# Kernel optimization log

Measured on AMD Instinct MI355X. Metric: run time of the kernel, lower is better.

The kernel has to match this reference:

```python
import jax, jax.numpy as jnp
import numpy as np

H = 2  # attention heads, concat=False -> mean over heads

def _gat(x, src, dst, eattr, W, a_s, a_d, We, a_e, b, N):
    # x: [N, Fin], W: [Fin, H*C], a_*: [H, C], We: [1, H*C], b: [C]
    C = W.shape[1] // H
    xh = (x @ W).reshape(N, H, C)                      # [N,H,C]
    al_s = jnp.einsum('nhc,hc->nh', xh, a_s)           # [N,H]
    al_d = jnp.einsum('nhc,hc->nh', xh, a_d)           # [N,H]
    eh = (eattr @ We).reshape(-1, H, C)                # [E,H,C]
    al_e = jnp.einsum('ehc,hc->eh', eh, a_e)           # [E,H]
    alpha = jax.nn.leaky_relu(al_s[src] + al_d[dst] + al_e, 0.2)
    # segment softmax over incoming edges of each dst node
    amax = jax.lax.stop_gradient(jax.ops.segment_max(alpha, dst, num_segments=N))
    ex = jnp.exp(alpha - amax[dst])
    den = jax.ops.segment_sum(ex, dst, num_segments=N)
    att = ex / (den[dst] + 1e-16)                      # [E,H]
    out = jax.ops.segment_sum(xh[src] * att[:, :, None], dst, num_segments=N)
    return out.mean(axis=1) + b                        # [N,C]


def setup_inputs() -> dict:
    key = jax.random.key(0)
    ks = jax.random.split(key, 24)
    N, E, Fin, Ch, NG = 50000, 800000, 5, 64, 64
    p = lambda k, shp: (jax.random.normal(k, shp, dtype=jnp.float32) * 0.1)
    inp = {
        'x': jax.random.normal(ks[0], (N, Fin), dtype=jnp.float32),
        'edge_index': jax.random.randint(ks[1], (2, E), 0, N),
        'edge_attr': jax.random.uniform(ks[2], (E, 1), dtype=jnp.float32),
        'batch': jnp.sort(jax.random.randint(ks[3], (N,), 0, NG)),
        'W1': p(ks[4], (Fin, H * Ch)), 'as1': p(ks[5], (H, Ch)), 'ad1': p(ks[6], (H, Ch)),
        'We1': p(ks[7], (1, H * Ch)), 'ae1': p(ks[8], (H, Ch)), 'b1': jnp.zeros((Ch,), jnp.float32),
        'W2': p(ks[9], (Ch, H * Ch)), 'as2': p(ks[10], (H, Ch)), 'ad2': p(ks[11], (H, Ch)),
        'We2': p(ks[12], (1, H * Ch)), 'ae2': p(ks[13], (H, Ch)), 'b2': jnp.zeros((Ch,), jnp.float32),
        'Wlin': p(ks[14], (Ch, 1)), 'blin': jnp.zeros((1,), jnp.float32),
    }
    return inp


def reference(x, edge_index, edge_attr, batch,
              W1, as1, ad1, We1, ae1, b1,
              W2, as2, ad2, We2, ae2, b2,
              Wlin, blin):
    N = x.shape[0]
    NG = 64
    src0, dst0 = edge_index[0], edge_index[1]
    # PyG GATConv add_self_loops=True, fill_value='mean': per-dst mean of edge_attr
    cnt = jax.ops.segment_sum(jnp.ones((src0.shape[0], 1), x.dtype), dst0, num_segments=N)
    loop_attr = jax.ops.segment_sum(edge_attr, dst0, num_segments=N) / jnp.maximum(cnt, 1.0)
    loops = jnp.arange(N)
    src = jnp.concatenate([src0, loops])
    dst = jnp.concatenate([dst0, loops])
    eattr = jnp.concatenate([edge_attr, loop_attr], axis=0)
    h = jax.nn.relu(_gat(x, src, dst, eattr, W1, as1, ad1, We1, ae1, b1, N))
    h = jax.nn.relu(_gat(h, src, dst, eattr, W2, as2, ad2, We2, ae2, b2, N))
    # global mean pool over graphs
    cntb = jax.ops.segment_sum(jnp.ones((N,), h.dtype), batch, num_segments=NG)
    pooled = jax.ops.segment_sum(h, batch, num_segments=NG) / jnp.maximum(cntb, 1.0)[:, None]
    return (pooled @ Wlin + blin).squeeze()
```

## Files before the change

kernel.cpp:

```cpp
#include <hip/hip_runtime.h>
#include <hip/hip_bf16.h>
#include <math.h>

typedef unsigned int u32;
typedef __attribute__((ext_vector_type(8))) short short8v;
typedef __attribute__((ext_vector_type(4))) float f32x4;

#define LRELU(a) ((a) > 0.f ? (a) : 0.2f * (a))

#define FIX_SCALE 67108864.0f
#define FIX_INV   (1.0f / 67108864.0f)
#define CNT_SHIFT 40
#define SUM_MASK  0xFFFFFFFFFFULL

__device__ __forceinline__ u32 f2bf(float f) {
    u32 u = __float_as_uint(f);
    return (u + 0x7fffu + ((u >> 16) & 1u)) >> 16;
}
__device__ __forceinline__ float bfl(u32 w) { return __uint_as_float(w << 16); }
__device__ __forceinline__ float bfh(u32 w) { return __uint_as_float(w & 0xffff0000u); }

#define RED(x) _Pragma("unroll") for (int m_ = 32; m_ >= 1; m_ >>= 1) x += __shfl_xor(x, m_);
#define REDMAX(x) _Pragma("unroll") for (int m_ = 32; m_ >= 1; m_ >>= 1) x = fmaxf(x, __shfl_xor(x, m_));
#define RED32(x) _Pragma("unroll") for (int m_ = 16; m_ >= 1; m_ >>= 1) x += __shfl_xor(x, m_);
#define REDMAX32(x) _Pragma("unroll") for (int m_ = 16; m_ >= 1; m_ >>= 1) x = fmaxf(x, __shfl_xor(x, m_));


__global__ void hist_pos_kernel(const int* __restrict__ dst, const float* __restrict__ eattr,
                                unsigned long long* __restrict__ hist, int* __restrict__ pos, int E) {
    int e = blockIdx.x * blockDim.x + threadIdx.x;
    if (e < E) {
        int d = dst[e];
        unsigned long long v = (1ULL << CNT_SHIFT) |
                               (unsigned long long)(eattr[e] * FIX_SCALE + 0.5f);
        unsigned long long old = atomicAdd(&hist[d], v);
        pos[e] = (int)(old >> CNT_SHIFT);
    }
}

__global__ __launch_bounds__(256) void scan_phase1(const unsigned long long* __restrict__ hist,
                                                   int* __restrict__ block_sum, int N) {
    int t = threadIdx.x;
    int n = blockIdx.x * 256 + t;
    int v = (n < N) ? (int)(hist[n] >> CNT_SHIFT) + 1 : 0;
    RED(v)
    __shared__ int ws[4];
    if ((t & 63) == 0) ws[t >> 6] = v;
    __syncthreads();
    if (t == 0) block_sum[blockIdx.x] = ws[0] + ws[1] + ws[2] + ws[3];
}

__global__ __launch_bounds__(1024) void scan_phase2(const int* __restrict__ block_sum,
                                                    int* __restrict__ block_off,
                                                    int* __restrict__ row_ptr, int B, int N) {
    __shared__ int s[1024];
    int t = threadIdx.x;
    int v = (t < B) ? block_sum[t] : 0;
    s[t] = v;
    __syncthreads();
    for (int off = 1; off < 1024; off <<= 1) {
        int u = (t >= off) ? s[t - off] : 0;
        __syncthreads();
        s[t] += u;
        __syncthreads();
    }
    if (t < B) block_off[t] = s[t] - v;
    if (t == 1023) row_ptr[N] = s[1023];
}

__global__ __launch_bounds__(256) void scan_phase3(const unsigned long long* __restrict__ hist,
                                                   const int* __restrict__ block_off,
                                                   int* __restrict__ row_ptr,
                                                   int2* __restrict__ col, int N) {
    int t = threadIdx.x;
    int lane = t & 63;
    int n = blockIdx.x * 256 + t;
    unsigned long long hv = (n < N) ? hist[n] : 0ULL;
    int c = (n < N) ? (int)(hv >> CNT_SHIFT) + 1 : 0;
    int v = c;
#pragma unroll
    for (int m = 1; m < 64; m <<= 1) {
        int u = __shfl_up(v, m);
        if (lane >= m) v += u;
    }
    __shared__ int wsum[4];
    if (lane == 63) wsum[t >> 6] = v;
    __syncthreads();
    int w = t >> 6;
    int wadd = 0;
#pragma unroll
    for (int i = 0; i < 3; i++) wadd += (i < w) ? wsum[i] : 0;
    int base = block_off[blockIdx.x] + wadd + v - c;
    if (n < N) {
        row_ptr[n] = base;
        float asum = (float)(hv & SUM_MASK) * FIX_INV;
        float la = asum / fmaxf((float)(c - 1), 1.f);
        col[base] = make_int2(n, __float_as_int(la));
    }
}

__global__ void place_kernel(const int* __restrict__ src, const int* __restrict__ dst,
                             const float* __restrict__ eattr, const int* __restrict__ row_ptr,
                             const int* __restrict__ pos, int2* __restrict__ col, int E) {
    int e = blockIdx.x * blockDim.x + threadIdx.x;
    if (e < E) {
        int d = dst[e];
        col[row_ptr[d] + 1 + pos[e]] = make_int2(src[e], __float_as_int(eattr[e]));
    }
}


__global__ __launch_bounds__(256) void prep2_kernel(
        const float* __restrict__ W1, const float* __restrict__ as1, const float* __restrict__ ad1,
        const float* __restrict__ We1, const float* __restrict__ ae1,
        const float* __restrict__ W2, const float* __restrict__ as2, const float* __restrict__ ad2,
        const float* __restrict__ We2, const float* __restrict__ ae2,
        float* __restrict__ wp, unsigned short* __restrict__ W2b) {
    int t = threadIdx.x;
    int g = t >> 6, lane = t & 63;
    const float* We = (g & 2) ? We2 : We1;
    const float* ae = (g & 2) ? ae2 : ae1;
    int h = g & 1;
    float v = We[h * 64 + lane] * ae[h * 64 + lane];
    RED(v)
    if (lane == 0) wp[g] = v;
    if (t < 20) {
        int dd = t / 10;
        int hh = (t % 10) / 5, k = t % 5;
        const float* a = dd ? ad1 : as1;
        float s = 0.f;
        for (int c = 0; c < 64; c++) s += W1[k * 128 + hh * 64 + c] * a[hh * 64 + c];
        wp[4 + dd * 10 + hh * 5 + k] = s;
    }
    {
        int dd = t >> 7;
        int hh = (t >> 6) & 1, k = t & 63;
        const float* a = dd ? ad2 : as2;
        float s = 0.f;
        for (int c = 0; c < 64; c++) s += W2[k * 128 + hh * 64 + c] * a[hh * 64 + c];
        wp[24 + dd * 128 + hh * 64 + k] = s;
    }
    for (int i = t; i < 128 * 64; i += 256) {
        int k = i >> 6, c = i & 63;
        W2b[i] = (unsigned short)f2bf(0.5f * W2[(k & 63) * 128 + (k & 64) + c]);
    }
}


__global__ __launch_bounds__(256) void node_pre1(
        const float* __restrict__ x, const float* __restrict__ wp,
        float2* __restrict__ al_s, float2* __restrict__ al_d, uint4* __restrict__ xb1, int N) {
    int n = blockIdx.x * 256 + threadIdx.x;
    if (n >= N) return;
    float f[5];
#pragma unroll
    for (int k = 0; k < 5; k++) f[k] = x[(size_t)n * 5 + k];
    float s0 = 0.f, s1 = 0.f, d0 = 0.f, d1 = 0.f;
#pragma unroll
    for (int k = 0; k < 5; k++) {
        s0 += f[k] * wp[4 + k];   s1 += f[k] * wp[9 + k];
        d0 += f[k] * wp[14 + k];  d1 += f[k] * wp[19 + k];
    }
    al_s[n] = make_float2(s0, s1);
    al_d[n] = make_float2(d0, d1);
    uint4 p;
    p.x = (f2bf(f[1]) << 16) | f2bf(f[0]);
    p.y = (f2bf(f[3]) << 16) | f2bf(f[2]);
    p.z = f2bf(f[4]);
    p.w = 0;
    xb1[n] = p;
}


__global__ __launch_bounds__(256) void edge_proj_L1(
        const int* __restrict__ row_ptr, const int2* __restrict__ col,
        const float2* __restrict__ al_s, const float2* __restrict__ al_d,
        const uint4* __restrict__ xb1, const float* __restrict__ wp,
        const float* __restrict__ W1, const float* __restrict__ b1,
        float2* __restrict__ al_s2, float2* __restrict__ al_d2, u32* __restrict__ xb2, int N) {
    int slane = threadIdx.x & 31;
    int n = blockIdx.x * 8 + (threadIdx.x >> 5);
    if (n >= N) return;
    int start = row_ptr[n], end = row_ptr[n + 1];
    int cnt = end - start;
    float we0 = wp[0], we1 = wp[1];
    float2 ald = al_d[n];
    float a00 = 0.f, a01 = 0.f, a02 = 0.f, a03 = 0.f, a04 = 0.f;
    float a10 = 0.f, a11 = 0.f, a12 = 0.f, a13 = 0.f, a14 = 0.f;
    float den0 = 0.f, den1 = 0.f;

    if (cnt <= 32) {
        float v0 = -INFINITY, v1 = -INFINITY;
        int sc = 0;
        if (slane < cnt) {
            int2 ce = col[start + slane];
            sc = ce.x;
            float at = __int_as_float(ce.y);
            float2 als = al_s[sc];
            v0 = LRELU(als.x + ald.x + we0 * at);
            v1 = LRELU(als.y + ald.y + we1 * at);
        }
        float m0 = v0, m1 = v1;
        REDMAX32(m0) REDMAX32(m1)
        if (slane < cnt) {
            float e0 = __expf(v0 - m0), e1 = __expf(v1 - m1);
            uint4 p = xb1[sc];
            float f0 = bfl(p.x), f1 = bfh(p.x), f2 = bfl(p.y), f3 = bfh(p.y), f4 = bfl(p.z);
            a00 = e0 * f0; a01 = e0 * f1; a02 = e0 * f2; a03 = e0 * f3; a04 = e0 * f4;
            a10 = e1 * f0; a11 = e1 * f1; a12 = e1 * f2; a13 = e1 * f3; a14 = e1 * f4;
            den0 = e0; den1 = e1;
        }
    } else {
        float m0 = -INFINITY, m1 = -INFINITY;
        for (int i = start + slane; i < end; i += 32) {
            int2 ce = col[i];
            float at = __int_as_float(ce.y);
            float2 als = al_s[ce.x];
            m0 = fmaxf(m0, LRELU(als.x + ald.x + we0 * at));
            m1 = fmaxf(m1, LRELU(als.y + ald.y + we1 * at));
        }
        REDMAX32(m0) REDMAX32(m1)
        for (int i = start + slane; i < end; i += 32) {
            int2 ce = col[i];
            float at = __int_as_float(ce.y);
            float2 als = al_s[ce.x];
            float e0 = __expf(LRELU(als.x + ald.x + we0 * at) - m0);
            float e1 = __expf(LRELU(als.y + ald.y + we1 * at) - m1);
            uint4 p = xb1[ce.x];
            float f0 = bfl(p.x), f1 = bfh(p.x), f2 = bfl(p.y), f3 = bfh(p.y), f4 = bfl(p.z);
            a00 += e0 * f0; a01 += e0 * f1; a02 += e0 * f2; a03 += e0 * f3; a04 += e0 * f4;
            a10 += e1 * f0; a11 += e1 * f1; a12 += e1 * f2; a13 += e1 * f3; a14 += e1 * f4;
            den0 += e0; den1 += e1;
        }
    }
    RED32(a00) RED32(a01) RED32(a02) RED32(a03) RED32(a04)
    RED32(a10) RED32(a11) RED32(a12) RED32(a13) RED32(a14)
    RED32(den0) RED32(den1)

    float i0 = 1.f / (den0 + 1e-16f), i1 = 1.f / (den1 + 1e-16f);
    float ag0[5] = {a00 * i0, a01 * i0, a02 * i0, a03 * i0, a04 * i0};
    float ag1[5] = {a10 * i1, a11 * i1, a12 * i1, a13 * i1, a14 * i1};
    const float2* W1v = (const float2*)W1;
    float s0 = 0.f, t0 = 0.f, s1 = 0.f, t1 = 0.f;
#pragma unroll
    for (int k = 0; k < 5; k++) {
        float2 w0 = W1v[k * 64 + slane];
        float2 w1 = W1v[k * 64 + 32 + slane];
        s0 += ag0[k] * w0.x; t0 += ag0[k] * w0.y;
        s1 += ag1[k] * w1.x; t1 += ag1[k] * w1.y;
    }
    float2 bb = ((const float2*)b1)[slane];
    float h0 = fmaxf(0.5f * (s0 + s1) + bb.x, 0.f);
    float h1 = fmaxf(0.5f * (t0 + t1) + bb.y, 0.f);

    float2 wa = ((const float2*)(wp + 24))[slane];
    float2 wb = ((const float2*)(wp + 88))[slane];
    float2 wc = ((const float2*)(wp + 152))[slane];
    float2 wd = ((const float2*)(wp + 216))[slane];
    float r0 = h0 * wa.x + h1 * wa.y;
    float r1 = h0 * wb.x + h1 * wb.y;
    float r2 = h0 * wc.x + h1 * wc.y;
    float r3 = h0 * wd.x + h1 * wd.y;
    RED32(r0) RED32(r1) RED32(r2) RED32(r3)
    if (slane == 0) {
        al_s2[n] = make_float2(r0, r1);
        al_d2[n] = make_float2(r2, r3);
    }
    xb2[(size_t)n * 32 + slane] = (f2bf(h1) << 16) | f2bf(h0);
}


__global__ __launch_bounds__(256) void edge_aggr_L2(
        const int* __restrict__ row_ptr, const int2* __restrict__ col,
        const float2* __restrict__ al_s, const float2* __restrict__ al_d,
        const u32* __restrict__ xb2, const float* __restrict__ wp,
        u32* __restrict__ agg2b, int N) {
    __shared__ float s_e0[8][32], s_e1[8][32];
    __shared__ int s_src[8][32];
    int seg = threadIdx.x >> 5;
    int slane = threadIdx.x & 31;
    int n = blockIdx.x * 8 + seg;
    if (n >= N) return;
    int start = row_ptr[n], end = row_ptr[n + 1];
    int cnt = end - start;
    float we0 = wp[2], we1 = wp[3];
    float2 ald = al_d[n];
    float ax0 = 0.f, ay0 = 0.f, ax1 = 0.f, ay1 = 0.f, den0 = 0.f, den1 = 0.f;

    if (cnt <= 32) {
        float v0 = -INFINITY, v1 = -INFINITY;
        int sc = 0;
        if (slane < cnt) {
            int2 ce = col[start + slane];
            sc = ce.x;
            float at = __int_as_float(ce.y);
            float2 als = al_s[sc];
            v0 = LRELU(als.x + ald.x + we0 * at);
            v1 = LRELU(als.y + ald.y + we1 * at);
        }
        float m0 = v0, m1 = v1;
        REDMAX32(m0) REDMAX32(m1)
        float e0 = 0.f, e1 = 0.f;
        if (slane < cnt) {
            e0 = __expf(v0 - m0);
            e1 = __expf(v1 - m1);
        }
        den0 = e0; den1 = e1;
        s_e0[seg][slane] = e0; s_e1[seg][slane] = e1; s_src[seg][slane] = sc;

#pragma unroll 4
        for (int j = 0; j < cnt; j++) {
            float w0 = s_e0[seg][j], w1 = s_e1[seg][j];
            u32 v = xb2[(size_t)s_src[seg][j] * 32 + slane];
            float lo = bfl(v), hi = bfh(v);
            ax0 += w0 * lo; ay0 += w0 * hi;
            ax1 += w1 * lo; ay1 += w1 * hi;
        }
    } else {
        float m0 = -INFINITY, m1 = -INFINITY;
        for (int i = start + slane; i < end; i += 32) {
            int2 ce = col[i];
            float at = __int_as_float(ce.y);
            float2 als = al_s[ce.x];
            m0 = fmaxf(m0, LRELU(als.x + ald.x + we0 * at));
            m1 = fmaxf(m1, LRELU(als.y + ald.y + we1 * at));
        }
        REDMAX32(m0) REDMAX32(m1)
        for (int cs = start; cs < end; cs += 32) {
            int i = cs + slane;
            float e0 = 0.f, e1 = 0.f;
            int sc = 0;
            if (i < end) {
                int2 ce = col[i];
                sc = ce.x;
                float at = __int_as_float(ce.y);
                float2 als = al_s[sc];
                e0 = __expf(LRELU(als.x + ald.x + we0 * at) - m0);
                e1 = __expf(LRELU(als.y + ald.y + we1 * at) - m1);
            }
            den0 += e0; den1 += e1;
            s_e0[seg][slane] = e0; s_e1[seg][slane] = e1; s_src[seg][slane] = sc;
            int c2 = min(32, end - cs);
#pragma unroll 4
            for (int j = 0; j < c2; j++) {
                float w0 = s_e0[seg][j], w1 = s_e1[seg][j];
                u32 v = xb2[(size_t)s_src[seg][j] * 32 + slane];
                float lo = bfl(v), hi = bfh(v);
                ax0 += w0 * lo; ay0 += w0 * hi;
                ax1 += w1 * lo; ay1 += w1 * hi;
            }
        }
    }
    RED32(den0) RED32(den1)
    float i0 = 1.f / (den0 + 1e-16f), i1 = 1.f / (den1 + 1e-16f);
    agg2b[(size_t)n * 64 + slane]      = (f2bf(ay0 * i0) << 16) | f2bf(ax0 * i0);
    agg2b[(size_t)n * 64 + 32 + slane] = (f2bf(ay1 * i1) << 16) | f2bf(ax1 * i1);
}


__global__ __launch_bounds__(256) void proj2_pool_mfma(
        const u32* __restrict__ agg2b, const unsigned short* __restrict__ W2b,
        const float* __restrict__ b2, const float* __restrict__ Wlin,
        const int* __restrict__ batch,
        float* __restrict__ pool_sum, int* __restrict__ pool_cnt, int N) {
    __shared__ float s_sum[64];
    __shared__ int s_cnt[64];
    int t = threadIdx.x;
    int wid = t >> 6, lane = t & 63;
    if (t < 64) { s_sum[t] = 0.f; s_cnt[t] = 0; }
    __syncthreads();

    int sub = lane >> 4, cc = lane & 15;

    short8v bfrag[4][4];
#pragma unroll
    for (int tl = 0; tl < 4; tl++)
#pragma unroll
        for (int kk = 0; kk < 4; kk++)
#pragma unroll
            for (int r = 0; r < 8; r++)
                bfrag[tl][kk][r] = (short)W2b[(kk * 32 + 8 * sub + r) * 64 + tl * 16 + cc];

    float b2v[4], wlv[4];
#pragma unroll
    for (int tl = 0; tl < 4; tl++) {
        b2v[tl] = b2[tl * 16 + cc];
        wlv[tl] = Wlin[tl * 16 + cc];
    }

    int nstrips = (N + 15) >> 4;
    for (int strip = blockIdx.x * 4 + wid; strip < nstrips; strip += gridDim.x * 4) {
        int n0 = strip << 4;
        int arow = min(n0 + cc, N - 1);
        const uint4* ap = (const uint4*)agg2b;
        short8v a[4];
#pragma unroll
        for (int kk = 0; kk < 4; kk++) {
            uint4 raw = ap[(size_t)arow * 16 + kk * 4 + sub];
            a[kk] = *(const short8v*)&raw;
        }

        f32x4 acc0 = {0.f, 0.f, 0.f, 0.f}, acc1 = acc0, acc2 = acc0, acc3 = acc0;
#pragma unroll
        for (int kk = 0; kk < 4; kk++) {
            acc0 = __builtin_amdgcn_mfma_f32_16x16x32_bf16(a[kk], bfrag[0][kk], acc0, 0, 0, 0);
            acc1 = __builtin_amdgcn_mfma_f32_16x16x32_bf16(a[kk], bfrag[1][kk], acc1, 0, 0, 0);
            acc2 = __builtin_amdgcn_mfma_f32_16x16x32_bf16(a[kk], bfrag[2][kk], acc2, 0, 0, 0);
            acc3 = __builtin_amdgcn_mfma_f32_16x16x32_bf16(a[kk], bfrag[3][kk], acc3, 0, 0, 0);
        }

#pragma unroll
        for (int r = 0; r < 4; r++) {
            float p = fmaxf(acc0[r] + b2v[0], 0.f) * wlv[0]
                    + fmaxf(acc1[r] + b2v[1], 0.f) * wlv[1]
                    + fmaxf(acc2[r] + b2v[2], 0.f) * wlv[2]
                    + fmaxf(acc3[r] + b2v[3], 0.f) * wlv[3];
#pragma unroll
            for (int m = 8; m >= 1; m >>= 1) p += __shfl_xor(p, m);
            if (cc == 0) {
                int node = n0 + sub * 4 + r;
                if (node < N) {
                    int g = batch[node];
                    atomicAdd(&s_sum[g], p);
                    atomicAdd(&s_cnt[g], 1);
                }
            }
        }
    }
    __syncthreads();
    if (t < 64 && s_cnt[t] > 0) {
        atomicAdd(&pool_sum[t], s_sum[t]);
        atomicAdd(&pool_cnt[t], s_cnt[t]);
    }
}

__global__ void final_kernel(const float* __restrict__ pool_sum, const int* __restrict__ pool_cnt,
                             const float* __restrict__ blin, float* __restrict__ out) {
    int g = threadIdx.x;
    if (g < 64) out[g] = pool_sum[g] / fmaxf((float)pool_cnt[g], 1.f) + blin[0];
}


extern "C" void kernel_launch(void* const* d_in, const int* in_sizes, int n_in,
                              void* d_out, int out_size, void* d_ws, size_t ws_size,
                              hipStream_t stream) {
    const float* x     = (const float*)d_in[0];
    const int*   ei    = (const int*)d_in[1];
    const float* eattr = (const float*)d_in[2];
    const int*   batch = (const int*)d_in[3];
    const float* W1  = (const float*)d_in[4];
    const float* as1 = (const float*)d_in[5];
    const float* ad1 = (const float*)d_in[6];
    const float* We1 = (const float*)d_in[7];
    const float* ae1 = (const float*)d_in[8];
    const float* b1  = (const float*)d_in[9];
    const float* W2  = (const float*)d_in[10];
    const float* as2 = (const float*)d_in[11];
    const float* ad2 = (const float*)d_in[12];
    const float* We2 = (const float*)d_in[13];
    const float* ae2 = (const float*)d_in[14];
    const float* b2  = (const float*)d_in[15];
    const float* Wlin = (const float*)d_in[16];
    const float* blin = (const float*)d_in[17];
    float* out = (float*)d_out;

    int N = in_sizes[0] / 5;
    int E = in_sizes[1] / 2;
    size_t EP = (size_t)E + N;
    const int* src0 = ei;
    const int* dst0 = ei + E;
    int B = (N + 255) / 256;

    char* ws = (char*)d_ws;
    size_t off = 0;
    auto alloc = [&](size_t bytes) {
        void* p = ws + off;
        off = (off + bytes + 255) & ~(size_t)255;
        return p;
    };
    unsigned long long* hist = (unsigned long long*)alloc((size_t)N * 8);
    int*    row_ptr  = (int*)   alloc((size_t)(N + 1) * 4);
    int*    pos      = (int*)   alloc((size_t)E * 4);
    int2*   col      = (int2*)  alloc(EP * 8);
    int*    block_sum= (int*)   alloc((size_t)1024 * 4);
    int*    block_off= (int*)   alloc((size_t)1024 * 4);
    float*  wp       = (float*) alloc(280 * 4);
    unsigned short* W2b = (unsigned short*)alloc((size_t)128 * 64 * 2);
    float2* al_s1    = (float2*)alloc((size_t)N * 8);
    float2* al_d1    = (float2*)alloc((size_t)N * 8);
    uint4*  xb1      = (uint4*) alloc((size_t)N * 16);
    float2* al_s2    = (float2*)alloc((size_t)N * 8);
    float2* al_d2    = (float2*)alloc((size_t)N * 8);
    u32*    xb2      = (u32*)   alloc((size_t)N * 32 * 4);
    u32*    agg2b    = (u32*)   alloc((size_t)N * 64 * 4);
    float*  pool_sum = (float*) alloc(64 * 4);
    int*    pool_cnt = (int*)   alloc(64 * 4);

    hipMemsetAsync(hist, 0, (size_t)N * 8, stream);
    hipMemsetAsync(block_sum, 0, (size_t)1024 * 4, stream);
    hipMemsetAsync(pool_sum, 0, 64 * 4, stream);
    hipMemsetAsync(pool_cnt, 0, 64 * 4, stream);

    hist_pos_kernel<<<(E + 255) / 256, 256, 0, stream>>>(dst0, eattr, hist, pos, E);
    scan_phase1<<<B, 256, 0, stream>>>(hist, block_sum, N);
    scan_phase2<<<1, 1024, 0, stream>>>(block_sum, block_off, row_ptr, B, N);
    scan_phase3<<<B, 256, 0, stream>>>(hist, block_off, row_ptr, col, N);
    place_kernel<<<(E + 255) / 256, 256, 0, stream>>>(src0, dst0, eattr, row_ptr, pos, col, E);
    prep2_kernel<<<1, 256, 0, stream>>>(W1, as1, ad1, We1, ae1, W2, as2, ad2, We2, ae2, wp, W2b);

    int eab8 = (N + 7) / 8;

    node_pre1<<<B, 256, 0, stream>>>(x, wp, al_s1, al_d1, xb1, N);
    edge_proj_L1<<<eab8, 256, 0, stream>>>(row_ptr, col, al_s1, al_d1, xb1, wp, W1, b1,
                                           al_s2, al_d2, xb2, N);
    edge_aggr_L2<<<eab8, 256, 0, stream>>>(row_ptr, col, al_s2, al_d2, xb2, wp, agg2b, N);
    int nstrips = (N + 15) / 16;
    proj2_pool_mfma<<<(nstrips + 3) / 4, 256, 0, stream>>>(agg2b, W2b, b2, Wlin, batch,
                                                           pool_sum, pool_cnt, N);
    final_kernel<<<1, 64, 0, stream>>>(pool_sum, pool_cnt, blin, out);
}
```

Baseline: 152.2 us.

## Fuse prep kernels, merge memsets, and drop softmax max-subtraction pass

Merges the histogram kernel with weight preprocessing and the scan phase-1 kernel with node pre-projection, so fewer kernels are launched. It also collapses four memsets into one by placing the zeroed buffers next to each other, and removes the block_sum memset. Separately, both edge kernels drop the segment-max pass and compute exp directly on the leaky-relu logits, removing a gather pass over edges and the warp max reductions. Skipping the max subtraction risks overflow or precision loss if the logits grow large; with these small weights that is unlikely but not guaranteed for general inputs.

```diff
diff --git a/kernel.cpp b/kernel.cpp
--- a/kernel.cpp
+++ b/kernel.cpp
@@ -21,102 +21,30 @@
 __device__ __forceinline__ float bfh(u32 w) { return __uint_as_float(w & 0xffff0000u); }
 
 #define RED(x) _Pragma("unroll") for (int m_ = 32; m_ >= 1; m_ >>= 1) x += __shfl_xor(x, m_);
-#define REDMAX(x) _Pragma("unroll") for (int m_ = 32; m_ >= 1; m_ >>= 1) x = fmaxf(x, __shfl_xor(x, m_));
 #define RED32(x) _Pragma("unroll") for (int m_ = 16; m_ >= 1; m_ >>= 1) x += __shfl_xor(x, m_);
-#define REDMAX32(x) _Pragma("unroll") for (int m_ = 16; m_ >= 1; m_ >>= 1) x = fmaxf(x, __shfl_xor(x, m_));
-
-
-__global__ void hist_pos_kernel(const int* __restrict__ dst, const float* __restrict__ eattr,
-                                unsigned long long* __restrict__ hist, int* __restrict__ pos, int E) {
-    int e = blockIdx.x * blockDim.x + threadIdx.x;
-    if (e < E) {
-        int d = dst[e];
-        unsigned long long v = (1ULL << CNT_SHIFT) |
-                               (unsigned long long)(eattr[e] * FIX_SCALE + 0.5f);
-        unsigned long long old = atomicAdd(&hist[d], v);
-        pos[e] = (int)(old >> CNT_SHIFT);
-    }
-}
-
-__global__ __launch_bounds__(256) void scan_phase1(const unsigned long long* __restrict__ hist,
-                                                   int* __restrict__ block_sum, int N) {
+
+
+__global__ void hist_prep_kernel(const int* __restrict__ dst, const float* __restrict__ eattr,
+                                 unsigned long long* __restrict__ hist, int* __restrict__ pos, int E,
+                                 const float* __restrict__ W1, const float* __restrict__ as1,
+                                 const float* __restrict__ ad1, const float* __restrict__ We1,
+                                 const float* __restrict__ ae1,
+                                 const float* __restrict__ W2, const float* __restrict__ as2,
+                                 const float* __restrict__ ad2, const float* __restrict__ We2,
+                                 const float* __restrict__ ae2,
+                                 float* __restrict__ wp, unsigned short* __restrict__ W2b, int HB) {
     int t = threadIdx.x;
-    int n = blockIdx.x * 256 + t;
-    int v = (n < N) ? (int)(hist[n] >> CNT_SHIFT) + 1 : 0;
-    RED(v)
-    __shared__ int ws[4];
-    if ((t & 63) == 0) ws[t >> 6] = v;
-    __syncthreads();
-    if (t == 0) block_sum[blockIdx.x] = ws[0] + ws[1] + ws[2] + ws[3];
-}
-
-__global__ __launch_bounds__(1024) void scan_phase2(const int* __restrict__ block_sum,
-                                                    int* __restrict__ block_off,
-                                                    int* __restrict__ row_ptr, int B, int N) {
-    __shared__ int s[1024];
-    int t = threadIdx.x;
-    int v = (t < B) ? block_sum[t] : 0;
-    s[t] = v;
-    __syncthreads();
-    for (int off = 1; off < 1024; off <<= 1) {
-        int u = (t >= off) ? s[t - off] : 0;
-        __syncthreads();
-        s[t] += u;
-        __syncthreads();
-    }
-    if (t < B) block_off[t] = s[t] - v;
-    if (t == 1023) row_ptr[N] = s[1023];
-}
-
-__global__ __launch_bounds__(256) void scan_phase3(const unsigned long long* __restrict__ hist,
-                                                   const int* __restrict__ block_off,
-                                                   int* __restrict__ row_ptr,
-                                                   int2* __restrict__ col, int N) {
-    int t = threadIdx.x;
-    int lane = t & 63;
-    int n = blockIdx.x * 256 + t;
-    unsigned long long hv = (n < N) ? hist[n] : 0ULL;
-    int c = (n < N) ? (int)(hv >> CNT_SHIFT) + 1 : 0;
-    int v = c;
-#pragma unroll
-    for (int m = 1; m < 64; m <<= 1) {
-        int u = __shfl_up(v, m);
-        if (lane >= m) v += u;
-    }
-    __shared__ int wsum[4];
-    if (lane == 63) wsum[t >> 6] = v;
-    __syncthreads();
-    int w = t >> 6;
-    int wadd = 0;
-#pragma unroll
-    for (int i = 0; i < 3; i++) wadd += (i < w) ? wsum[i] : 0;
-    int base = block_off[blockIdx.x] + wadd + v - c;
-    if (n < N) {
-        row_ptr[n] = base;
-        float asum = (float)(hv & SUM_MASK) * FIX_INV;
-        float la = asum / fmaxf((float)(c - 1), 1.f);
-        col[base] = make_int2(n, __float_as_int(la));
-    }
-}
-
-__global__ void place_kernel(const int* __restrict__ src, const int* __restrict__ dst,
-                             const float* __restrict__ eattr, const int* __restrict__ row_ptr,
-                             const int* __restrict__ pos, int2* __restrict__ col, int E) {
-    int e = blockIdx.x * blockDim.x + threadIdx.x;
-    if (e < E) {
-        int d = dst[e];
-        col[row_ptr[d] + 1 + pos[e]] = make_int2(src[e], __float_as_int(eattr[e]));
-    }
-}
-
-
-__global__ __launch_bounds__(256) void prep2_kernel(
-        const float* __restrict__ W1, const float* __restrict__ as1, const float* __restrict__ ad1,
-        const float* __restrict__ We1, const float* __restrict__ ae1,
-        const float* __restrict__ W2, const float* __restrict__ as2, const float* __restrict__ ad2,
-        const float* __restrict__ We2, const float* __restrict__ ae2,
-        float* __restrict__ wp, unsigned short* __restrict__ W2b) {
-    int t = threadIdx.x;
+    if ((int)blockIdx.x < HB) {
+        int e = blockIdx.x * 256 + t;
+        if (e < E) {
+            int d = dst[e];
+            unsigned long long v = (1ULL << CNT_SHIFT) |
+                                   (unsigned long long)(eattr[e] * FIX_SCALE + 0.5f);
+            unsigned long long old = atomicAdd(&hist[d], v);
+            pos[e] = (int)(old >> CNT_SHIFT);
+        }
+        return;
+    }
     int g = t >> 6, lane = t & 63;
     const float* We = (g & 2) ? We2 : We1;
     const float* ae = (g & 2) ? ae2 : ae1;
@@ -147,10 +75,22 @@
 }
 
 
-__global__ __launch_bounds__(256) void node_pre1(
+__global__ __launch_bounds__(256) void scan1_pre_kernel(
+        const unsigned long long* __restrict__ hist, int* __restrict__ block_sum, int N, int B,
         const float* __restrict__ x, const float* __restrict__ wp,
-        float2* __restrict__ al_s, float2* __restrict__ al_d, uint4* __restrict__ xb1, int N) {
-    int n = blockIdx.x * 256 + threadIdx.x;
+        float2* __restrict__ al_s, float2* __restrict__ al_d, uint4* __restrict__ xb1) {
+    int t = threadIdx.x;
+    if ((int)blockIdx.x < B) {
+        int n = blockIdx.x * 256 + t;
+        int v = (n < N) ? (int)(hist[n] >> CNT_SHIFT) + 1 : 0;
+        RED(v)
+        __shared__ int ws[4];
+        if ((t & 63) == 0) ws[t >> 6] = v;
+        __syncthreads();
+        if (t == 0) block_sum[blockIdx.x] = ws[0] + ws[1] + ws[2] + ws[3];
+        return;
+    }
+    int n = (blockIdx.x - B) * 256 + t;
     if (n >= N) return;
     float f[5];
 #pragma unroll
@@ -169,6 +109,65 @@
     p.z = f2bf(f[4]);
     p.w = 0;
     xb1[n] = p;
+}
+
+__global__ __launch_bounds__(1024) void scan_phase2(const int* __restrict__ block_sum,
+                                                    int* __restrict__ block_off,
+                                                    int* __restrict__ row_ptr, int B, int N) {
+    __shared__ int s[1024];
+    int t = threadIdx.x;
+    int v = (t < B) ? block_sum[t] : 0;
+    s[t] = v;
+    __syncthreads();
+    for (int off = 1; off < 1024; off <<= 1) {
+        int u = (t >= off) ? s[t - off] : 0;
+        __syncthreads();
+        s[t] += u;
+        __syncthreads();
+    }
+    if (t < B) block_off[t] = s[t] - v;
+    if (t == 1023) row_ptr[N] = s[1023];
+}
+
+__global__ __launch_bounds__(256) void scan_phase3(const unsigned long long* __restrict__ hist,
+                                                   const int* __restrict__ block_off,
+                                                   int* __restrict__ row_ptr,
+                                                   int2* __restrict__ col, int N) {
+    int t = threadIdx.x;
+    int lane = t & 63;
+    int n = blockIdx.x * 256 + t;
+    unsigned long long hv = (n < N) ? hist[n] : 0ULL;
+    int c = (n < N) ? (int)(hv >> CNT_SHIFT) + 1 : 0;
+    int v = c;
+#pragma unroll
+    for (int m = 1; m < 64; m <<= 1) {
+        int u = __shfl_up(v, m);
+        if (lane >= m) v += u;
+    }
+    __shared__ int wsum[4];
+    if (lane == 63) wsum[t >> 6] = v;
+    __syncthreads();
+    int w = t >> 6;
+    int wadd = 0;
+#pragma unroll
+    for (int i = 0; i < 3; i++) wadd += (i < w) ? wsum[i] : 0;
+    int base = block_off[blockIdx.x] + wadd + v - c;
+    if (n < N) {
+        row_ptr[n] = base;
+        float asum = (float)(hv & SUM_MASK) * FIX_INV;
+        float la = asum / fmaxf((float)(c - 1), 1.f);
+        col[base] = make_int2(n, __float_as_int(la));
+    }
+}
+
+__global__ void place_kernel(const int* __restrict__ src, const int* __restrict__ dst,
+                             const float* __restrict__ eattr, const int* __restrict__ row_ptr,
+                             const int* __restrict__ pos, int2* __restrict__ col, int E) {
+    int e = blockIdx.x * blockDim.x + threadIdx.x;
+    if (e < E) {
+        int d = dst[e];
+        col[row_ptr[d] + 1 + pos[e]] = make_int2(src[e], __float_as_int(eattr[e]));
+    }
 }
 
 
@@ -190,20 +189,13 @@
     float den0 = 0.f, den1 = 0.f;
 
     if (cnt <= 32) {
-        float v0 = -INFINITY, v1 = -INFINITY;
-        int sc = 0;
         if (slane < cnt) {
             int2 ce = col[start + slane];
-            sc = ce.x;
+            int sc = ce.x;
             float at = __int_as_float(ce.y);
             float2 als = al_s[sc];
-            v0 = LRELU(als.x + ald.x + we0 * at);
-            v1 = LRELU(als.y + ald.y + we1 * at);
-        }
-        float m0 = v0, m1 = v1;
-        REDMAX32(m0) REDMAX32(m1)
-        if (slane < cnt) {
-            float e0 = __expf(v0 - m0), e1 = __expf(v1 - m1);
+            float e0 = __expf(LRELU(als.x + ald.x + we0 * at));
+            float e1 = __expf(LRELU(als.y + ald.y + we1 * at));
             uint4 p = xb1[sc];
             float f0 = bfl(p.x), f1 = bfh(p.x), f2 = bfl(p.y), f3 = bfh(p.y), f4 = bfl(p.z);
             a00 = e0 * f0; a01 = e0 * f1; a02 = e0 * f2; a03 = e0 * f3; a04 = e0 * f4;
@@ -211,21 +203,12 @@
             den0 = e0; den1 = e1;
         }
     } else {
-        float m0 = -INFINITY, m1 = -INFINITY;
         for (int i = start + slane; i < end; i += 32) {
             int2 ce = col[i];
             float at = __int_as_float(ce.y);
             float2 als = al_s[ce.x];
-            m0 = fmaxf(m0, LRELU(als.x + ald.x + we0 * at));
-            m1 = fmaxf(m1, LRELU(als.y + ald.y + we1 * at));
-        }
-        REDMAX32(m0) REDMAX32(m1)
-        for (int i = start + slane; i < end; i += 32) {
-            int2 ce = col[i];
-            float at = __int_as_float(ce.y);
-            float2 als = al_s[ce.x];
-            float e0 = __expf(LRELU(als.x + ald.x + we0 * at) - m0);
-            float e1 = __expf(LRELU(als.y + ald.y + we1 * at) - m1);
+            float e0 = __expf(LRELU(als.x + ald.x + we0 * at));
+            float e1 = __expf(LRELU(als.y + ald.y + we1 * at));
             uint4 p = xb1[ce.x];
             float f0 = bfl(p.x), f1 = bfh(p.x), f2 = bfl(p.y), f3 = bfh(p.y), f4 = bfl(p.z);
             a00 += e0 * f0; a01 += e0 * f1; a02 += e0 * f2; a03 += e0 * f3; a04 += e0 * f4;
@@ -288,22 +271,15 @@
     float ax0 = 0.f, ay0 = 0.f, ax1 = 0.f, ay1 = 0.f, den0 = 0.f, den1 = 0.f;
 
     if (cnt <= 32) {
-        float v0 = -INFINITY, v1 = -INFINITY;
+        float e0 = 0.f, e1 = 0.f;
         int sc = 0;
         if (slane < cnt) {
             int2 ce = col[start + slane];
             sc = ce.x;
             float at = __int_as_float(ce.y);
             float2 als = al_s[sc];
-            v0 = LRELU(als.x + ald.x + we0 * at);
-            v1 = LRELU(als.y + ald.y + we1 * at);
-        }
-        float m0 = v0, m1 = v1;
-        REDMAX32(m0) REDMAX32(m1)
-        float e0 = 0.f, e1 = 0.f;
-        if (slane < cnt) {
-            e0 = __expf(v0 - m0);
-            e1 = __expf(v1 - m1);
+            e0 = __expf(LRELU(als.x + ald.x + we0 * at));
+            e1 = __expf(LRELU(als.y + ald.y + we1 * at));
         }
         den0 = e0; den1 = e1;
         s_e0[seg][slane] = e0; s_e1[seg][slane] = e1; s_src[seg][slane] = sc;
@@ -317,15 +293,6 @@
             ax1 += w1 * lo; ay1 += w1 * hi;
         }
     } else {
-        float m0 = -INFINITY, m1 = -INFINITY;
-        for (int i = start + slane; i < end; i += 32) {
-            int2 ce = col[i];
-            float at = __int_as_float(ce.y);
-            float2 als = al_s[ce.x];
-            m0 = fmaxf(m0, LRELU(als.x + ald.x + we0 * at));
-            m1 = fmaxf(m1, LRELU(als.y + ald.y + we1 * at));
-        }
-        REDMAX32(m0) REDMAX32(m1)
         for (int cs = start; cs < end; cs += 32) {
             int i = cs + slane;
             float e0 = 0.f, e1 = 0.f;
@@ -335,8 +302,8 @@
                 sc = ce.x;
                 float at = __int_as_float(ce.y);
                 float2 als = al_s[sc];
-                e0 = __expf(LRELU(als.x + ald.x + we0 * at) - m0);
-                e1 = __expf(LRELU(als.y + ald.y + we1 * at) - m1);
+                e0 = __expf(LRELU(als.x + ald.x + we0 * at));
+                e1 = __expf(LRELU(als.y + ald.y + we1 * at));
             }
             den0 += e0; den1 += e1;
             s_e0[seg][slane] = e0; s_e1[seg][slane] = e1; s_src[seg][slane] = sc;
@@ -470,6 +437,7 @@
     const int* src0 = ei;
     const int* dst0 = ei + E;
     int B = (N + 255) / 256;
+    int HB = (E + 255) / 256;
 
     char* ws = (char*)d_ws;
     size_t off = 0;
@@ -479,6 +447,9 @@
         return p;
     };
     unsigned long long* hist = (unsigned long long*)alloc((size_t)N * 8);
+    float*  pool_sum = (float*) alloc(64 * 4);
+    int*    pool_cnt = (int*)   alloc(64 * 4);
+    size_t zero_bytes = off;
     int*    row_ptr  = (int*)   alloc((size_t)(N + 1) * 4);
     int*    pos      = (int*)   alloc((size_t)E * 4);
     int2*   col      = (int2*)  alloc(EP * 8);
@@ -493,24 +464,20 @@
     float2* al_d2    = (float2*)alloc((size_t)N * 8);
     u32*    xb2      = (u32*)   alloc((size_t)N * 32 * 4);
     u32*    agg2b    = (u32*)   alloc((size_t)N * 64 * 4);
-    float*  pool_sum = (float*) alloc(64 * 4);
-    int*    pool_cnt = (int*)   alloc(64 * 4);
-
-    hipMemsetAsync(hist, 0, (size_t)N * 8, stream);
-    hipMemsetAsync(block_sum, 0, (size_t)1024 * 4, stream);
-    hipMemsetAsync(pool_sum, 0, 64 * 4, stream);
-    hipMemsetAsync(pool_cnt, 0, 64 * 4, stream);
-
-    hist_pos_kernel<<<(E + 255) / 256, 256, 0, stream>>>(dst0, eattr, hist, pos, E);
-    scan_phase1<<<B, 256, 0, stream>>>(hist, block_sum, N);
+
+    hipMemsetAsync(hist, 0, zero_bytes, stream);
+
+    hist_prep_kernel<<<HB + 1, 256, 0, stream>>>(dst0, eattr, hist, pos, E,
+                                                 W1, as1, ad1, We1, ae1,
+                                                 W2, as2, ad2, We2, ae2, wp, W2b, HB);
+    scan1_pre_kernel<<<2 * B, 256, 0, stream>>>(hist, block_sum, N, B, x, wp,
+                                                al_s1, al_d1, xb1);
     scan_phase2<<<1, 1024, 0, stream>>>(block_sum, block_off, row_ptr, B, N);
     scan_phase3<<<B, 256, 0, stream>>>(hist, block_off, row_ptr, col, N);
-    place_kernel<<<(E + 255) / 256, 256, 0, stream>>>(src0, dst0, eattr, row_ptr, pos, col, E);
-    prep2_kernel<<<1, 256, 0, stream>>>(W1, as1, ad1, We1, ae1, W2, as2, ad2, We2, ae2, wp, W2b);
+    place_kernel<<<HB, 256, 0, stream>>>(src0, dst0, eattr, row_ptr, pos, col, E);
 
     int eab8 = (N + 7) / 8;
 
-    node_pre1<<<B, 256, 0, stream>>>(x, wp, al_s1, al_d1, xb1, N);
     edge_proj_L1<<<eab8, 256, 0, stream>>>(row_ptr, col, al_s1, al_d1, xb1, wp, W1, b1,
                                            al_s2, al_d2, xb2, N);
     edge_aggr_L2<<<eab8, 256, 0, stream>>>(row_ptr, col, al_s2, al_d2, xb2, wp, agg2b, N);
```

New measurement: 136.7 us. 10.2% less time.
